# Optimization experiments

Measured on AMD Instinct MI355X. Metric: run time of the kernel, lower is better.

## Reference

```python
import jax, jax.numpy as jnp
import numpy as np

N, E, F, H, L, G = 100000, 1600000, 32, 64, 4, 256
EPS = 1e-5


def setup_inputs() -> dict:
    key = jax.random.key(0)
    ks = jax.random.split(key, 12)
    x = jax.random.normal(ks[0], (N, F), dtype=jnp.float32)
    edge_index = jax.random.randint(ks[1], (2, E), 0, N, dtype=jnp.int32)
    batch = jnp.sort(jax.random.randint(ks[2], (N,), 0, G, dtype=jnp.int32))
    s = 0.1
    return {
        "x": x,
        "edge_index": edge_index,
        "batch": batch,
        "w_embed": jax.random.normal(ks[3], (F, H), dtype=jnp.float32) * s,
        "b_embed": jnp.zeros((H,), dtype=jnp.float32),
        "conv_W": jax.random.normal(ks[4], (L, H, H), dtype=jnp.float32) * s,
        "conv_b": jnp.zeros((L, H), dtype=jnp.float32),
        "bn_gamma": jnp.ones((L, H), dtype=jnp.float32),
        "bn_beta": jnp.zeros((L, H), dtype=jnp.float32),
        "w1": jax.random.normal(ks[5], (H, H // 2), dtype=jnp.float32) * s,
        "b1": jnp.zeros((H // 2,), dtype=jnp.float32),
        "w2": jax.random.normal(ks[6], (H // 2, 1), dtype=jnp.float32) * s,
        "b2": jnp.zeros((1,), dtype=jnp.float32),
    }


def _gcn_conv(h, src, dst, W, b):
    # PyG GCNConv: add self loops, symmetric D^-1/2 (A+I) D^-1/2 normalization
    hw = h @ W  # [N,H]
    deg = jax.ops.segment_sum(jnp.ones((E,), h.dtype), dst, num_segments=N) + 1.0
    dinv = jax.lax.rsqrt(deg)  # [N]
    msg = hw[src] * (dinv[src] * dinv[dst])[:, None]  # [E,H] gather + scale
    agg = jax.ops.segment_sum(msg, dst, num_segments=N)  # scatter-add
    agg = agg + hw * (dinv * dinv)[:, None]  # self-loop contribution
    return agg + b


def _batchnorm(h, gamma, beta):
    # training-mode BatchNorm1d over the node dimension
    mean = jnp.mean(h, axis=0)
    var = jnp.var(h, axis=0)
    return (h - mean) * jax.lax.rsqrt(var + EPS) * gamma + beta


def reference(x, edge_index, batch, w_embed, b_embed, conv_W, conv_b,
              bn_gamma, bn_beta, w1, b1, w2, b2):
    src, dst = edge_index[0], edge_index[1]
    h = x @ w_embed + b_embed  # node embedding [N,H]
    for i in range(L):
        identity = h
        h = _gcn_conv(h, src, dst, conv_W[i], conv_b[i])
        h = _batchnorm(h, bn_gamma[i], bn_beta[i])
        h = jax.nn.relu(h)
        # dropout is identity in eval mode
        h = h + identity  # use_residual=True
    # global mean pool over graphs
    sums = jax.ops.segment_sum(h, batch, num_segments=G)  # [G,H]
    counts = jax.ops.segment_sum(jnp.ones((N,), h.dtype), batch, num_segments=G)
    pooled = sums / jnp.maximum(counts, 1.0)[:, None]
    out = jax.nn.relu(pooled @ w1 + b1)
    out = out @ w2 + b2  # [G,1]
    return out
```

## Files before the change

### kernel.cpp

```cpp
#include <hip/hip_runtime.h>
#include <hip/hip_fp16.h>

#define Nn 100000
#define Ne 1600000
#define Fi 32
#define Hd 64
#define Ll 4
#define Gg 256
#define BN_EPS 1e-5f
#define NPB 128
#define NBINS ((Nn + NPB - 1) / NPB)
#define CHUNK 4096
#define NBLK ((Ne + CHUNK - 1) / CHUNK)
#define IDXW (NBINS + 2)
#define TPAD 68
#define XPAD 36
#define NGB ((Nn + 63) / 64)
#define NSH 128
#define WSZ 256


__global__ void k_scanA(const int* __restrict__ deg, int* __restrict__ row_off,
                        int* __restrict__ bsum) {
    __shared__ int s[256];
    int t = threadIdx.x;
    int i = blockIdx.x * 256 + t;
    int v = (i < Nn) ? deg[i] : 0;
    s[t] = v;
    __syncthreads();
    int x = v;
    for (int off = 1; off < 256; off <<= 1) {
        int u = (t >= off) ? s[t - off] : 0;
        __syncthreads();
        x += u;
        s[t] = x;
        __syncthreads();
    }
    if (i < Nn) row_off[i] = x - v;
    if (t == 255) bsum[blockIdx.x] = x;
}

__global__ void k_scanBG(int* __restrict__ bsum, int nblk,
                         const int* __restrict__ batch, int* __restrict__ gstart) {
    int t = threadIdx.x;
    if (blockIdx.x == 1) {
        if (t < Gg) {
            int lo = 0, hi = Nn;
            while (lo < hi) {
                int mid = (lo + hi) >> 1;
                if (batch[mid] < t) lo = mid + 1; else hi = mid;
            }
            gstart[t] = lo;
            if (t == 0) gstart[Gg] = Nn;
        }
        return;
    }
    __shared__ int s[512];
    int v = (t < nblk) ? bsum[t] : 0;
    s[t] = v;
    __syncthreads();
    int x = v;
    for (int off = 1; off < 512; off <<= 1) {
        int u = (t >= off) ? s[t - off] : 0;
        __syncthreads();
        x += u;
        s[t] = x;
        __syncthreads();
    }
    if (t < nblk) bsum[t] = x - v;
}

__global__ void k_scanC(int* __restrict__ row_off, const int* __restrict__ bsum,
                        const int* __restrict__ deg, float* __restrict__ dinv) {
    int i = blockIdx.x * 256 + threadIdx.x;
    if (i < Nn) {
        row_off[i] += bsum[blockIdx.x];
        dinv[i] = rsqrtf((float)deg[i] + 1.0f);
    }
    if (i == 0) row_off[Nn] = Ne;
}

__global__ __launch_bounds__(256) void k_part(const int* __restrict__ src,
                                              const int* __restrict__ dst,
                                              unsigned* __restrict__ tpack,
                                              unsigned short* __restrict__ idx16) {
    __shared__ int hist[NBINS];
    __shared__ int lofs[NBINS + 1];
    __shared__ int wsum[256];
    __shared__ unsigned stage[CHUNK];
    int blk = blockIdx.x, t = threadIdx.x;
    int e0 = blk * CHUNK;
    int nval = min(CHUNK, Ne - e0);

    for (int i = t; i < NBINS; i += 256) hist[i] = 0;
    __syncthreads();
    for (int i = t; i < nval; i += 256)
        atomicAdd(&hist[dst[e0 + i] >> 7], 1);
    __syncthreads();

    int base = t * 4;
    int loc[4];
    int s = 0;
#pragma unroll
    for (int k = 0; k < 4; k++) {
        int b = base + k;
        int c = (b < NBINS) ? hist[b] : 0;
        loc[k] = s;
        s += c;
    }
    wsum[t] = s;
    __syncthreads();
    int x = s;
    for (int off = 1; off < 256; off <<= 1) {
        int u = (t >= off) ? wsum[t - off] : 0;
        __syncthreads();
        x += u;
        wsum[t] = x;
        __syncthreads();
    }
    int excl = x - s;
#pragma unroll
    for (int k = 0; k < 4; k++) {
        int b = base + k;
        if (b < NBINS) lofs[b] = excl + loc[k];
    }
    if (t == 0) lofs[NBINS] = nval;
    __syncthreads();

    for (int i = t; i <= NBINS; i += 256)
        idx16[(size_t)blk * IDXW + i] = (unsigned short)lofs[i];

    for (int i = t; i < NBINS; i += 256) hist[i] = lofs[i];
    __syncthreads();
    for (int i = t; i < nval; i += 256) {
        int d = dst[e0 + i];
        int sv = src[e0 + i];
        int p = atomicAdd(&hist[d >> 7], 1);
        stage[p] = (unsigned)sv | ((unsigned)(d & (NPB - 1)) << 17);
    }
    __syncthreads();
    for (int i = t; i < nval; i += 256)
        tpack[(size_t)blk * CHUNK + i] = stage[i];
}

__global__ __launch_bounds__(256) void k_deg2(const unsigned* __restrict__ tpack,
                                              const unsigned short* __restrict__ idx16,
                                              int* __restrict__ deg) {
    __shared__ int cnt[NPB];
    int b = blockIdx.x, t = threadIdx.x;
    if (t < NPB) cnt[t] = 0;
    __syncthreads();
    for (int r = t; r < NBLK; r += 256) {
        const unsigned short* row = idx16 + (size_t)r * IDXW;
        int s = row[b], e = row[b + 1];
        const unsigned* tp = tpack + (size_t)r * CHUNK;
        for (int k = s; k < e; k++)
            atomicAdd(&cnt[tp[k] >> 17], 1);
    }
    __syncthreads();
    int node = b * NPB + t;
    if (t < NPB && node < Nn) deg[node] = cnt[t];
}

__global__ __launch_bounds__(256) void k_csr(const int* __restrict__ row_off,
                                             const unsigned* __restrict__ tpack,
                                             const unsigned short* __restrict__ idx16,
                                             int* __restrict__ esrc) {
    __shared__ int cur[NPB];
    int b = blockIdx.x, t = threadIdx.x;
    int n0 = b * NPB;
    int e0 = row_off[n0];
    if (t < NPB) {
        int node = n0 + t;
        cur[t] = (node < Nn) ? (row_off[node] - e0) : 0;
    }
    __syncthreads();
    for (int r = t; r < NBLK; r += 256) {
        const unsigned short* row = idx16 + (size_t)r * IDXW;
        int s = row[b], e = row[b + 1];
        const unsigned* tp = tpack + (size_t)r * CHUNK;
        for (int k = s; k < e; k++) {
            unsigned v = tp[k];
            int p = atomicAdd(&cur[v >> 17], 1);
            esrc[e0 + p] = (int)(v & 0x1FFFFu);
        }
    }
}


#define MT_FMA(AV, W0, W1, W2, W3, R)                                          \
    acc[R][0] = fmaf(AV.x, W0.x, acc[R][0]);                                   \
    acc[R][0] = fmaf(AV.y, W1.x, acc[R][0]);                                   \
    acc[R][0] = fmaf(AV.z, W2.x, acc[R][0]);                                   \
    acc[R][0] = fmaf(AV.w, W3.x, acc[R][0]);                                   \
    acc[R][1] = fmaf(AV.x, W0.y, acc[R][1]);                                   \
    acc[R][1] = fmaf(AV.y, W1.y, acc[R][1]);                                   \
    acc[R][1] = fmaf(AV.z, W2.y, acc[R][1]);                                   \
    acc[R][1] = fmaf(AV.w, W3.y, acc[R][1]);                                   \
    acc[R][2] = fmaf(AV.x, W0.z, acc[R][2]);                                   \
    acc[R][2] = fmaf(AV.y, W1.z, acc[R][2]);                                   \
    acc[R][2] = fmaf(AV.z, W2.z, acc[R][2]);                                   \
    acc[R][2] = fmaf(AV.w, W3.z, acc[R][2]);                                   \
    acc[R][3] = fmaf(AV.x, W0.w, acc[R][3]);                                   \
    acc[R][3] = fmaf(AV.y, W1.w, acc[R][3]);                                   \
    acc[R][3] = fmaf(AV.z, W2.w, acc[R][3]);                                   \
    acc[R][3] = fmaf(AV.w, W3.w, acc[R][3]);

__device__ inline void store_half4(unsigned short* dst, float a, float b,
                                   float c, float d) {
    __half2 p0 = __floats2half2_rn(a, b);
    __half2 p1 = __floats2half2_rn(c, d);
    uint2 u;
    u.x = *(unsigned*)&p0;
    u.y = *(unsigned*)&p1;
    *(uint2*)dst = u;
}

__global__ __launch_bounds__(256, 4) void k_gemmF2(const float* __restrict__ agg,
                                                   const float* __restrict__ bnacc,
                                                   const float* __restrict__ gamma,
                                                   const float* __restrict__ beta,
                                                   float* __restrict__ h,
                                                   const float* __restrict__ W,
                                                   const float* __restrict__ dinv,
                                                   unsigned short* __restrict__ hwh) {
    __shared__ float hs[64 * TPAD];
    __shared__ float ws[64 * 64];
    __shared__ float bsc[64], bsh[64];
    int t = threadIdx.x;
    int n0 = blockIdx.x * 64;

    for (int f = t; f < 1024; f += 256)
        ((float4*)ws)[f] = ((const float4*)W)[f];

    if (t < 64) {
        float s = 0.f, s2 = 0.f;
        for (int shd = 0; shd < NSH; shd++) {
            s  += bnacc[shd * 128 + t];
            s2 += bnacc[shd * 128 + 64 + t];
        }
        float mean = s / (float)Nn;
        float var = fmaxf(s2 / (float)Nn - mean * mean, 0.f);
        float scv = gamma[t] * rsqrtf(var + BN_EPS);
        bsc[t] = scv;
        bsh[t] = beta[t] - mean * scv;
    }
    __syncthreads();

    for (int f = t; f < 1024; f += 256) {
        int row = f >> 4, c4 = (f & 15) * 4;
        int node = n0 + row;
        if (node < Nn) {
            float4 a  = *(const float4*)(agg + (size_t)node * Hd + c4);
            float4 ho = *(const float4*)(h + (size_t)node * Hd + c4);
            float4 sc = ((const float4*)bsc)[f & 15];
            float4 sh = ((const float4*)bsh)[f & 15];
            float4 r4;
            r4.x = fmaxf(fmaf(a.x, sc.x, sh.x), 0.f) + ho.x;
            r4.y = fmaxf(fmaf(a.y, sc.y, sh.y), 0.f) + ho.y;
            r4.z = fmaxf(fmaf(a.z, sc.z, sh.z), 0.f) + ho.z;
            r4.w = fmaxf(fmaf(a.w, sc.w, sh.w), 0.f) + ho.w;
            *(float4*)(h + (size_t)node * Hd + c4) = r4;
            *(float4*)&hs[row * TPAD + c4] = r4;
        } else {
            *(float4*)&hs[row * TPAD + c4] = make_float4(0.f, 0.f, 0.f, 0.f);
        }
    }
    __syncthreads();

    int i = t >> 4, j = t & 15;
    float acc[4][4] = {};
#pragma unroll 2
    for (int k = 0; k < 64; k += 4) {
        float4 w0 = *(const float4*)&ws[(k + 0) * 64 + 4 * j];
        float4 w1 = *(const float4*)&ws[(k + 1) * 64 + 4 * j];
        float4 w2 = *(const float4*)&ws[(k + 2) * 64 + 4 * j];
        float4 w3 = *(const float4*)&ws[(k + 3) * 64 + 4 * j];
        float4 a0 = *(const float4*)&hs[(4 * i + 0) * TPAD + k];
        float4 a1 = *(const float4*)&hs[(4 * i + 1) * TPAD + k];
        float4 a2 = *(const float4*)&hs[(4 * i + 2) * TPAD + k];
        float4 a3 = *(const float4*)&hs[(4 * i + 3) * TPAD + k];
        MT_FMA(a0, w0, w1, w2, w3, 0)
        MT_FMA(a1, w0, w1, w2, w3, 1)
        MT_FMA(a2, w0, w1, w2, w3, 2)
        MT_FMA(a3, w0, w1, w2, w3, 3)
    }
#pragma unroll
    for (int r = 0; r < 4; r++) {
        int node = n0 + 4 * i + r;
        if (node < Nn) {
            float dv = dinv[node];
            store_half4(hwh + (size_t)node * Hd + 4 * j,
                        acc[r][0] * dv, acc[r][1] * dv, acc[r][2] * dv,
                        acc[r][3] * dv);
        }
    }
}

__global__ __launch_bounds__(256, 4) void k_embed_gemm2(const float* __restrict__ x,
                                                        const float* __restrict__ we,
                                                        const float* __restrict__ be,
                                                        const float* __restrict__ W,
                                                        float* __restrict__ h,
                                                        const float* __restrict__ dinv,
                                                        unsigned short* __restrict__ hwh) {
    __shared__ float uni[64 * XPAD + 32 * 64];
    __shared__ float hs[64 * TPAD];
    __shared__ float bes[64];
    float* xs  = uni;
    float* wes = uni + 64 * XPAD;
    float* ws  = uni;
    int t = threadIdx.x;
    int n0 = blockIdx.x * 64;

    for (int f = t; f < 512; f += 256)
        ((float4*)wes)[f] = ((const float4*)we)[f];
    if (t < 64) bes[t] = be[t];

    for (int f = t; f < 512; f += 256) {
        int row = f >> 3, c4 = (f & 7) * 4;
        int node = n0 + row;
        float4 v = (node < Nn) ? *(const float4*)(x + (size_t)node * Fi + c4)
                               : make_float4(0.f, 0.f, 0.f, 0.f);
        *(float4*)&xs[row * XPAD + c4] = v;
    }
    __syncthreads();

    int i = t >> 4, j = t & 15;
    {
        float acc[4][4];
#pragma unroll
        for (int r = 0; r < 4; r++)
#pragma unroll
            for (int c = 0; c < 4; c++) acc[r][c] = bes[4 * j + c];
#pragma unroll 2
        for (int k = 0; k < 32; k += 4) {
            float4 w0 = *(const float4*)&wes[(k + 0) * 64 + 4 * j];
            float4 w1 = *(const float4*)&wes[(k + 1) * 64 + 4 * j];
            float4 w2 = *(const float4*)&wes[(k + 2) * 64 + 4 * j];
            float4 w3 = *(const float4*)&wes[(k + 3) * 64 + 4 * j];
            float4 a0 = *(const float4*)&xs[(4 * i + 0) * XPAD + k];
            float4 a1 = *(const float4*)&xs[(4 * i + 1) * XPAD + k];
            float4 a2 = *(const float4*)&xs[(4 * i + 2) * XPAD + k];
            float4 a3 = *(const float4*)&xs[(4 * i + 3) * XPAD + k];
            MT_FMA(a0, w0, w1, w2, w3, 0)
            MT_FMA(a1, w0, w1, w2, w3, 1)
            MT_FMA(a2, w0, w1, w2, w3, 2)
            MT_FMA(a3, w0, w1, w2, w3, 3)
        }
#pragma unroll
        for (int r = 0; r < 4; r++) {
            int node = n0 + 4 * i + r;
            float4 hv = make_float4(acc[r][0], acc[r][1], acc[r][2], acc[r][3]);
            *(float4*)&hs[(4 * i + r) * TPAD + 4 * j] = hv;
            if (node < Nn)
                *(float4*)(h + (size_t)node * Hd + 4 * j) = hv;
        }
    }
    __syncthreads();
    for (int f = t; f < 1024; f += 256)
        ((float4*)ws)[f] = ((const float4*)W)[f];
    __syncthreads();
    {
        float acc[4][4] = {};
#pragma unroll 2
        for (int k = 0; k < 64; k += 4) {
            float4 w0 = *(const float4*)&ws[(k + 0) * 64 + 4 * j];
            float4 w1 = *(const float4*)&ws[(k + 1) * 64 + 4 * j];
            float4 w2 = *(const float4*)&ws[(k + 2) * 64 + 4 * j];
            float4 w3 = *(const float4*)&ws[(k + 3) * 64 + 4 * j];
            float4 a0 = *(const float4*)&hs[(4 * i + 0) * TPAD + k];
            float4 a1 = *(const float4*)&hs[(4 * i + 1) * TPAD + k];
            float4 a2 = *(const float4*)&hs[(4 * i + 2) * TPAD + k];
            float4 a3 = *(const float4*)&hs[(4 * i + 3) * TPAD + k];
            MT_FMA(a0, w0, w1, w2, w3, 0)
            MT_FMA(a1, w0, w1, w2, w3, 1)
            MT_FMA(a2, w0, w1, w2, w3, 2)
            MT_FMA(a3, w0, w1, w2, w3, 3)
        }
#pragma unroll
        for (int r = 0; r < 4; r++) {
            int node = n0 + 4 * i + r;
            if (node < Nn) {
                float dv = dinv[node];
                store_half4(hwh + (size_t)node * Hd + 4 * j,
                            acc[r][0] * dv, acc[r][1] * dv, acc[r][2] * dv,
                            acc[r][3] * dv);
            }
        }
    }
}


__global__ __launch_bounds__(256) void k_gatherH(const unsigned short* __restrict__ hwh,
                                                 const float* __restrict__ dinv,
                                                 const int* __restrict__ row_off,
                                                 const int* __restrict__ esrc,
                                                 const float* __restrict__ bias,
                                                 float* __restrict__ agg,
                                                 float* __restrict__ bnacc) {
    __shared__ int se[4][WSZ];
    __shared__ float ls[2048];
    int t = threadIdx.x;
    int w = t >> 6, lane = t & 63;
    int g = lane >> 3, l = lane & 7;
    int node = blockIdx.x * 32 + w * 8 + g;
    float di = dinv[node];
    int en0 = row_off[node], en1 = row_off[node + 1];
    int we0 = __shfl(en0, 0, 64);
    int we1 = __shfl(en1, 63, 64);

    float acc[8];
    uint4 v = *(const uint4*)(hwh + (size_t)node * Hd + l * 8);
#pragma unroll
    for (int q = 0; q < 4; q++) {
        float2 f = __half22float2(*(__half2*)(((unsigned*)&v) + q));
        acc[2 * q]     = f.x;
        acc[2 * q + 1] = f.y;
    }

    for (int wb = we0; wb < we1; wb += WSZ) {
        int cnt = min(WSZ, we1 - wb);
        for (int k2 = lane; k2 < cnt; k2 += 64)
            se[w][k2] = esrc[wb + k2];
        __builtin_amdgcn_wave_barrier();
        asm volatile("s_waitcnt lgkmcnt(0)" ::: "memory");
        int j  = max(en0, wb) - wb;
        int j1 = min(en1, wb + cnt) - wb;
        for (; j + 7 < j1; j += 8) {
            uint4 vv[8];
#pragma unroll
            for (int u = 0; u < 8; u++)
                vv[u] = *(const uint4*)(hwh + (size_t)se[w][j + u] * Hd + l * 8);
#pragma unroll
            for (int u = 0; u < 8; u++) {
#pragma unroll
                for (int q = 0; q < 4; q++) {
                    float2 f = __half22float2(*(__half2*)(((unsigned*)&vv[u]) + q));
                    acc[2 * q]     += f.x;
                    acc[2 * q + 1] += f.y;
                }
            }
        }
        for (; j < j1; j++) {
            uint4 v0 = *(const uint4*)(hwh + (size_t)se[w][j] * Hd + l * 8);
#pragma unroll
            for (int q = 0; q < 4; q++) {
                float2 f = __half22float2(*(__half2*)(((unsigned*)&v0) + q));
                acc[2 * q]     += f.x;
                acc[2 * q + 1] += f.y;
            }
        }
        __builtin_amdgcn_wave_barrier();
    }

#pragma unroll
    for (int q = 0; q < 8; q++)
        acc[q] = fmaf(acc[q], di, bias[l * 8 + q]);

    *(float4*)(agg + (size_t)node * Hd + l * 8)     = make_float4(acc[0], acc[1], acc[2], acc[3]);
    *(float4*)(agg + (size_t)node * Hd + l * 8 + 4) = make_float4(acc[4], acc[5], acc[6], acc[7]);

    int g32 = t >> 3;
    *(float4*)&ls[g32 * 64 + l * 8]     = make_float4(acc[0], acc[1], acc[2], acc[3]);
    *(float4*)&ls[g32 * 64 + l * 8 + 4] = make_float4(acc[4], acc[5], acc[6], acc[7]);
    __syncthreads();
    if (t < 64) {
        float s = 0.f, s2 = 0.f;
#pragma unroll
        for (int gg = 0; gg < 32; gg++) {
            float vv = ls[gg * 64 + t];
            s += vv;
            s2 = fmaf(vv, vv, s2);
        }
        float* a = bnacc + (blockIdx.x & (NSH - 1)) * 128;
        atomicAdd(&a[t], s);
        atomicAdd(&a[64 + t], s2);
    }
}

__global__ __launch_bounds__(1024) void k_poolF(const float* __restrict__ agg,
                                                const float* __restrict__ bnacc,
                                                const float* __restrict__ gamma,
                                                const float* __restrict__ beta,
                                                const float* __restrict__ h,
                                                const int* __restrict__ gstart,
                                                float* __restrict__ pooled) {
    __shared__ float ls[1024];
    __shared__ float bsc[64], bsh[64];
    int g = blockIdx.x;
    int t = threadIdx.x;
    if (t < 64) {
        float s = 0.f, s2 = 0.f;
        for (int shd = 0; shd < NSH; shd++) {
            s  += bnacc[shd * 128 + t];
            s2 += bnacc[shd * 128 + 64 + t];
        }
        float mean = s / (float)Nn;
        float var = fmaxf(s2 / (float)Nn - mean * mean, 0.f);
        float scv = gamma[t] * rsqrtf(var + BN_EPS);
        bsc[t] = scv;
        bsh[t] = beta[t] - mean * scv;
    }
    __syncthreads();
    int ch = t & 63, sl = t >> 6;
    float sc = bsc[ch], shv = bsh[ch];
    int n0 = gstart[g], n1 = gstart[g + 1];
    float s = 0.f;
    for (int n = n0 + sl; n < n1; n += 16) {
        float a  = agg[(size_t)n * Hd + ch];
        float ho = h[(size_t)n * Hd + ch];
        s += fmaxf(fmaf(a, sc, shv), 0.f) + ho;
    }
    ls[t] = s;
    __syncthreads();
    if (t < 64) {
        float acc = 0.f;
#pragma unroll
        for (int k = 0; k < 16; k++) acc += ls[k * 64 + t];
        float cnt = (float)(n1 - n0);
        pooled[g * Hd + t] = acc / fmaxf(cnt, 1.0f);
    }
}

__global__ __launch_bounds__(256) void k_head(const float* __restrict__ pooled,
                                              const float* __restrict__ w1,
                                              const float* __restrict__ b1,
                                              const float* __restrict__ w2,
                                              const float* __restrict__ b2,
                                              float* __restrict__ out) {
    __shared__ float sw1[Hd * 32], sw2[32], sb1[32];
    int t = threadIdx.x;
    for (int i = t; i < Hd * 32; i += 256) sw1[i] = w1[i];
    if (t < 32) { sw2[t] = w2[t]; sb1[t] = b1[t]; }
    __syncthreads();
    float acc2[32];
#pragma unroll
    for (int k = 0; k < 32; k++) acc2[k] = sb1[k];
    for (int j = 0; j < Hd; j++) {
        float pj = pooled[t * Hd + j];
#pragma unroll
        for (int k = 0; k < 32; k++) acc2[k] = fmaf(pj, sw1[j * 32 + k], acc2[k]);
    }
    float o = b2[0];
#pragma unroll
    for (int k = 0; k < 32; k++) o += fmaxf(acc2[k], 0.f) * sw2[k];
    out[t] = o;
}


extern "C" void kernel_launch(void* const* d_in, const int* in_sizes, int n_in,
                              void* d_out, int out_size, void* d_ws, size_t ws_size,
                              hipStream_t stream) {
    const float* x       = (const float*)d_in[0];
    const int*   eidx    = (const int*)d_in[1];
    const int*   batch   = (const int*)d_in[2];
    const float* w_embed = (const float*)d_in[3];
    const float* b_embed = (const float*)d_in[4];
    const float* conv_W  = (const float*)d_in[5];
    const float* conv_b  = (const float*)d_in[6];
    const float* gamma   = (const float*)d_in[7];
    const float* beta    = (const float*)d_in[8];
    const float* w1      = (const float*)d_in[9];
    const float* b1      = (const float*)d_in[10];
    const float* w2      = (const float*)d_in[11];
    const float* b2      = (const float*)d_in[12];
    const int* src = eidx;
    const int* dst = eidx + Ne;

    char* p = (char*)d_ws;
    auto alloc = [&](size_t bytes) -> void* {
        void* r = (void*)p;
        p += (bytes + 255) / 256 * 256;
        return r;
    };
    float*    h       = (float*)alloc((size_t)Nn * Hd * 4);
    unsigned short* hwh = (unsigned short*)alloc((size_t)Nn * Hd * 2);
    float*    agg     = (float*)alloc((size_t)Nn * Hd * 4);
    int*      deg     = (int*)alloc((size_t)Nn * 4);
    int*      row_off = (int*)alloc((size_t)(Nn + 1) * 4);
    float*    dinv    = (float*)alloc((size_t)Nn * 4);
    int*      bsum    = (int*)alloc(512 * 4);
    int*      esrc    = (int*)alloc((size_t)Ne * 4);
    unsigned* tpack   = (unsigned*)alloc((size_t)NBLK * CHUNK * 4);
    unsigned short* idx16 = (unsigned short*)alloc((size_t)NBLK * IDXW * 2);
    float*    bnacc   = (float*)alloc((size_t)Ll * NSH * 128 * 4);
    float*    pooled  = (float*)alloc((size_t)Gg * Hd * 4);
    int*      gstart  = (int*)alloc((size_t)(Gg + 1) * 4);
    (void)ws_size; (void)in_sizes; (void)n_in; (void)out_size;

    const int NB_N = (Nn + 255) / 256;
    const int NB_G32 = Nn / 32;

    hipMemsetAsync(bnacc, 0, (size_t)Ll * NSH * 128 * 4, stream);

    k_part<<<NBLK, 256, 0, stream>>>(src, dst, tpack, idx16);
    k_deg2<<<NBINS, 256, 0, stream>>>(tpack, idx16, deg);
    k_scanA<<<NB_N, 256, 0, stream>>>(deg, row_off, bsum);
    k_scanBG<<<2, 512, 0, stream>>>(bsum, NB_N, batch, gstart);
    k_scanC<<<NB_N, 256, 0, stream>>>(row_off, bsum, deg, dinv);
    k_csr<<<NBINS, 256, 0, stream>>>(row_off, tpack, idx16, esrc);

    k_embed_gemm2<<<NGB, 256, 0, stream>>>(x, w_embed, b_embed, conv_W, h, dinv, hwh);

    for (int i = 0; i < Ll; i++) {
        if (i > 0)
            k_gemmF2<<<NGB, 256, 0, stream>>>(agg, bnacc + (size_t)(i - 1) * NSH * 128,
                                              gamma + (size_t)(i - 1) * Hd,
                                              beta + (size_t)(i - 1) * Hd, h,
                                              conv_W + (size_t)i * Hd * Hd, dinv, hwh);
        k_gatherH<<<NB_G32, 256, 0, stream>>>(hwh, dinv, row_off, esrc,
                                              conv_b + (size_t)i * Hd, agg,
                                              bnacc + (size_t)i * NSH * 128);
    }

    k_poolF<<<Gg, 1024, 0, stream>>>(agg, bnacc + (size_t)(Ll - 1) * NSH * 128,
                                     gamma + (size_t)(Ll - 1) * Hd,
                                     beta + (size_t)(Ll - 1) * Hd, h, gstart, pooled);
    k_head<<<1, 256, 0, stream>>>(pooled, w1, b1, w2, b2, (float*)d_out);
}
```

Baseline: 346.4 us.

## Split hidden features into 16-wide slabs and gather each slab in a separate pass

```diff
diff --git a/kernel.cpp b/kernel.cpp
--- a/kernel.cpp
+++ b/kernel.cpp
@@ -17,7 +17,7 @@
 #define XPAD 36
 #define NGB ((Nn + 63) / 64)
 #define NSH 128
-#define WSZ 256
+#define NB_GQ ((Nn + 127) / 128)
 
 
 __global__ void k_scanA(const int* __restrict__ deg, int* __restrict__ row_off,
@@ -216,6 +216,10 @@
     *(uint2*)dst = u;
 }
 
+__device__ inline unsigned short* hwh_addr(unsigned short* hwh, int node, int j) {
+    return hwh + ((size_t)(j >> 2) * Nn + node) * 16 + 4 * (j & 3);
+}
+
 __global__ __launch_bounds__(256, 4) void k_gemmF2(const float* __restrict__ agg,
                                                    const float* __restrict__ bnacc,
                                                    const float* __restrict__ gamma,
@@ -290,7 +294,7 @@
         int node = n0 + 4 * i + r;
         if (node < Nn) {
             float dv = dinv[node];
-            store_half4(hwh + (size_t)node * Hd + 4 * j,
+            store_half4(hwh_addr(hwh, node, j),
                         acc[r][0] * dv, acc[r][1] * dv, acc[r][2] * dv,
                         acc[r][3] * dv);
         }
@@ -383,7 +387,7 @@
             int node = n0 + 4 * i + r;
             if (node < Nn) {
                 float dv = dinv[node];
-                store_half4(hwh + (size_t)node * Hd + 4 * j,
+                store_half4(hwh_addr(hwh, node, j),
                             acc[r][0] * dv, acc[r][1] * dv, acc[r][2] * dv,
                             acc[r][3] * dv);
             }
@@ -392,90 +396,79 @@
 }
 
 
-__global__ __launch_bounds__(256) void k_gatherH(const unsigned short* __restrict__ hwh,
+__global__ __launch_bounds__(256) void k_gather4(const unsigned short* __restrict__ hwq,
                                                  const float* __restrict__ dinv,
                                                  const int* __restrict__ row_off,
                                                  const int* __restrict__ esrc,
                                                  const float* __restrict__ bias,
                                                  float* __restrict__ agg,
-                                                 float* __restrict__ bnacc) {
-    __shared__ int se[4][WSZ];
-    __shared__ float ls[2048];
+                                                 float* __restrict__ bnacc,
+                                                 int q) {
+    __shared__ float ls[128 * 16];
     int t = threadIdx.x;
-    int w = t >> 6, lane = t & 63;
-    int g = lane >> 3, l = lane & 7;
-    int node = blockIdx.x * 32 + w * 8 + g;
-    float di = dinv[node];
-    int en0 = row_off[node], en1 = row_off[node + 1];
-    int we0 = __shfl(en0, 0, 64);
-    int we1 = __shfl(en1, 63, 64);
-
-    float acc[8];
-    uint4 v = *(const uint4*)(hwh + (size_t)node * Hd + l * 8);
-#pragma unroll
-    for (int q = 0; q < 4; q++) {
-        float2 f = __half22float2(*(__half2*)(((unsigned*)&v) + q));
-        acc[2 * q]     = f.x;
-        acc[2 * q + 1] = f.y;
-    }
-
-    for (int wb = we0; wb < we1; wb += WSZ) {
-        int cnt = min(WSZ, we1 - wb);
-        for (int k2 = lane; k2 < cnt; k2 += 64)
-            se[w][k2] = esrc[wb + k2];
-        __builtin_amdgcn_wave_barrier();
-        asm volatile("s_waitcnt lgkmcnt(0)" ::: "memory");
-        int j  = max(en0, wb) - wb;
-        int j1 = min(en1, wb + cnt) - wb;
-        for (; j + 7 < j1; j += 8) {
+    int slot = t >> 1, half = t & 1;
+    int node = blockIdx.x * 128 + slot;
+    float acc[8] = {0.f, 0.f, 0.f, 0.f, 0.f, 0.f, 0.f, 0.f};
+
+    if (node < Nn) {
+        float di = dinv[node];
+        uint4 v = *(const uint4*)(hwq + (size_t)node * 16 + half * 8);
+#pragma unroll
+        for (int k = 0; k < 4; k++) {
+            float2 f = __half22float2(*(__half2*)(((unsigned*)&v) + k));
+            acc[2 * k]     = f.x;
+            acc[2 * k + 1] = f.y;
+        }
+        int e = row_off[node], e1 = row_off[node + 1];
+        for (; e + 7 < e1; e += 8) {
             uint4 vv[8];
 #pragma unroll
             for (int u = 0; u < 8; u++)
-                vv[u] = *(const uint4*)(hwh + (size_t)se[w][j + u] * Hd + l * 8);
+                vv[u] = *(const uint4*)(hwq + (size_t)esrc[e + u] * 16 + half * 8);
 #pragma unroll
             for (int u = 0; u < 8; u++) {
 #pragma unroll
-                for (int q = 0; q < 4; q++) {
-                    float2 f = __half22float2(*(__half2*)(((unsigned*)&vv[u]) + q));
-                    acc[2 * q]     += f.x;
-                    acc[2 * q + 1] += f.y;
+                for (int k = 0; k < 4; k++) {
+                    float2 f = __half22float2(*(__half2*)(((unsigned*)&vv[u]) + k));
+                    acc[2 * k]     += f.x;
+                    acc[2 * k + 1] += f.y;
                 }
             }
         }
-        for (; j < j1; j++) {
-            uint4 v0 = *(const uint4*)(hwh + (size_t)se[w][j] * Hd + l * 8);
-#pragma unroll
-            for (int q = 0; q < 4; q++) {
-                float2 f = __half22float2(*(__half2*)(((unsigned*)&v0) + q));
-                acc[2 * q]     += f.x;
-                acc[2 * q + 1] += f.y;
+        for (; e < e1; e++) {
+            uint4 v0 = *(const uint4*)(hwq + (size_t)esrc[e] * 16 + half * 8);
+#pragma unroll
+            for (int k = 0; k < 4; k++) {
+                float2 f = __half22float2(*(__half2*)(((unsigned*)&v0) + k));
+                acc[2 * k]     += f.x;
+                acc[2 * k + 1] += f.y;
             }
         }
-        __builtin_amdgcn_wave_barrier();
-    }
-
-#pragma unroll
-    for (int q = 0; q < 8; q++)
-        acc[q] = fmaf(acc[q], di, bias[l * 8 + q]);
-
-    *(float4*)(agg + (size_t)node * Hd + l * 8)     = make_float4(acc[0], acc[1], acc[2], acc[3]);
-    *(float4*)(agg + (size_t)node * Hd + l * 8 + 4) = make_float4(acc[4], acc[5], acc[6], acc[7]);
-
-    int g32 = t >> 3;
-    *(float4*)&ls[g32 * 64 + l * 8]     = make_float4(acc[0], acc[1], acc[2], acc[3]);
-    *(float4*)&ls[g32 * 64 + l * 8 + 4] = make_float4(acc[4], acc[5], acc[6], acc[7]);
-    __syncthreads();
-    if (t < 64) {
+#pragma unroll
+        for (int k = 0; k < 8; k++)
+            acc[k] = fmaf(acc[k], di, bias[q * 16 + half * 8 + k]);
+        *(float4*)(agg + (size_t)node * Hd + q * 16 + half * 8)     =
+            make_float4(acc[0], acc[1], acc[2], acc[3]);
+        *(float4*)(agg + (size_t)node * Hd + q * 16 + half * 8 + 4) =
+            make_float4(acc[4], acc[5], acc[6], acc[7]);
+    } else {
+#pragma unroll
+        for (int k = 0; k < 8; k++) acc[k] = 0.f;
+    }
+
+    *(float4*)&ls[slot * 16 + half * 8]     = make_float4(acc[0], acc[1], acc[2], acc[3]);
+    *(float4*)&ls[slot * 16 + half * 8 + 4] = make_float4(acc[4], acc[5], acc[6], acc[7]);
+    __syncthreads();
+    if (t < 16) {
         float s = 0.f, s2 = 0.f;
-#pragma unroll
-        for (int gg = 0; gg < 32; gg++) {
-            float vv = ls[gg * 64 + t];
+        for (int n2 = 0; n2 < 128; n2++) {
+            float vv = ls[n2 * 16 + t];
             s += vv;
             s2 = fmaf(vv, vv, s2);
         }
         float* a = bnacc + (blockIdx.x & (NSH - 1)) * 128;
-        atomicAdd(&a[t], s);
-        atomicAdd(&a[64 + t], s2);
+        atomicAdd(&a[q * 16 + t], s);
+        atomicAdd(&a[64 + q * 16 + t], s2);
     }
 }
 
@@ -590,7 +583,6 @@
     (void)ws_size; (void)in_sizes; (void)n_in; (void)out_size;
 
     const int NB_N = (Nn + 255) / 256;
-    const int NB_G32 = Nn / 32;
 
     hipMemsetAsync(bnacc, 0, (size_t)Ll * NSH * 128 * 4, stream);
 
@@ -609,9 +601,11 @@
                                               gamma + (size_t)(i - 1) * Hd,
                                               beta + (size_t)(i - 1) * Hd, h,
                                               conv_W + (size_t)i * Hd * Hd, dinv, hwh);
-        k_gatherH<<<NB_G32, 256, 0, stream>>>(hwh, dinv, row_off, esrc,
-                                              conv_b + (size_t)i * Hd, agg,
-                                              bnacc + (size_t)i * NSH * 128);
+        for (int q = 0; q < 4; q++)
+            k_gather4<<<NB_GQ, 256, 0, stream>>>(hwh + (size_t)q * Nn * 16, dinv,
+                                                 row_off, esrc,
+                                                 conv_b + (size_t)i * Hd, agg,
+                                                 bnacc + (size_t)i * NSH * 128, q);
     }
 
     k_poolF<<<Gg, 1024, 0, stream>>>(agg, bnacc + (size_t)(Ll - 1) * NSH * 128,
```

Measured after the change: 519.0 us. +49.8%, slower.

## Store hidden state and aggregation buffers in fp16, simplify gather loop

Applied to the files above, without the earlier changes.

```diff
diff --git a/kernel.cpp b/kernel.cpp
--- a/kernel.cpp
+++ b/kernel.cpp
@@ -17,7 +17,6 @@
 #define XPAD 36
 #define NGB ((Nn + 63) / 64)
 #define NSH 128
-#define WSZ 256
 
 
 __global__ void k_scanA(const int* __restrict__ deg, int* __restrict__ row_off,
@@ -216,11 +215,29 @@
     *(uint2*)dst = u;
 }
 
-__global__ __launch_bounds__(256, 4) void k_gemmF2(const float* __restrict__ agg,
+__device__ inline void store_half8(unsigned short* dst, const float* a) {
+    __half2 p0 = __floats2half2_rn(a[0], a[1]);
+    __half2 p1 = __floats2half2_rn(a[2], a[3]);
+    __half2 p2 = __floats2half2_rn(a[4], a[5]);
+    __half2 p3 = __floats2half2_rn(a[6], a[7]);
+    uint4 u;
+    u.x = *(unsigned*)&p0; u.y = *(unsigned*)&p1;
+    u.z = *(unsigned*)&p2; u.w = *(unsigned*)&p3;
+    *(uint4*)dst = u;
+}
+
+__device__ inline float4 load_half4(const unsigned short* p) {
+    uint2 u = *(const uint2*)p;
+    float2 f0 = __half22float2(*(__half2*)&u.x);
+    float2 f1 = __half22float2(*(__half2*)&u.y);
+    return make_float4(f0.x, f0.y, f1.x, f1.y);
+}
+
+__global__ __launch_bounds__(256, 4) void k_gemmF2(const unsigned short* __restrict__ aggh,
                                                    const float* __restrict__ bnacc,
                                                    const float* __restrict__ gamma,
                                                    const float* __restrict__ beta,
-                                                   float* __restrict__ h,
+                                                   unsigned short* __restrict__ hh,
                                                    const float* __restrict__ W,
                                                    const float* __restrict__ dinv,
                                                    unsigned short* __restrict__ hwh) {
@@ -251,8 +268,8 @@
         int row = f >> 4, c4 = (f & 15) * 4;
         int node = n0 + row;
         if (node < Nn) {
-            float4 a  = *(const float4*)(agg + (size_t)node * Hd + c4);
-            float4 ho = *(const float4*)(h + (size_t)node * Hd + c4);
+            float4 a  = load_half4(aggh + (size_t)node * Hd + c4);
+            float4 ho = load_half4(hh + (size_t)node * Hd + c4);
             float4 sc = ((const float4*)bsc)[f & 15];
             float4 sh = ((const float4*)bsh)[f & 15];
             float4 r4;
@@ -260,7 +277,7 @@
             r4.y = fmaxf(fmaf(a.y, sc.y, sh.y), 0.f) + ho.y;
             r4.z = fmaxf(fmaf(a.z, sc.z, sh.z), 0.f) + ho.z;
             r4.w = fmaxf(fmaf(a.w, sc.w, sh.w), 0.f) + ho.w;
-            *(float4*)(h + (size_t)node * Hd + c4) = r4;
+            store_half4(hh + (size_t)node * Hd + c4, r4.x, r4.y, r4.z, r4.w);
             *(float4*)&hs[row * TPAD + c4] = r4;
         } else {
             *(float4*)&hs[row * TPAD + c4] = make_float4(0.f, 0.f, 0.f, 0.f);
@@ -301,7 +318,7 @@
                                                         const float* __restrict__ we,
                                                         const float* __restrict__ be,
                                                         const float* __restrict__ W,
-                                                        float* __restrict__ h,
+                                                        unsigned short* __restrict__ hh,
                                                         const float* __restrict__ dinv,
                                                         unsigned short* __restrict__ hwh) {
     __shared__ float uni[64 * XPAD + 32 * 64];
@@ -354,7 +371,7 @@
             float4 hv = make_float4(acc[r][0], acc[r][1], acc[r][2], acc[r][3]);
             *(float4*)&hs[(4 * i + r) * TPAD + 4 * j] = hv;
             if (node < Nn)
-                *(float4*)(h + (size_t)node * Hd + 4 * j) = hv;
+                store_half4(hh + (size_t)node * Hd + 4 * j, hv.x, hv.y, hv.z, hv.w);
         }
     }
     __syncthreads();
@@ -397,20 +414,14 @@
                                                  const int* __restrict__ row_off,
                                                  const int* __restrict__ esrc,
                                                  const float* __restrict__ bias,
-                                                 float* __restrict__ agg,
+                                                 unsigned short* __restrict__ aggh,
                                                  float* __restrict__ bnacc) {
-    __shared__ int se[4][WSZ];
-    __shared__ float ls[2048];
-    int t = threadIdx.x;
-    int w = t >> 6, lane = t & 63;
-    int g = lane >> 3, l = lane & 7;
-    int node = blockIdx.x * 32 + w * 8 + g;
+    int g = threadIdx.x >> 3;
+    int l = threadIdx.x & 7;
+    int node = blockIdx.x * 32 + g;
     float di = dinv[node];
-    int en0 = row_off[node], en1 = row_off[node + 1];
-    int we0 = __shfl(en0, 0, 64);
-    int we1 = __shfl(en1, 63, 64);
-
     float acc[8];
+
     uint4 v = *(const uint4*)(hwh + (size_t)node * Hd + l * 8);
 #pragma unroll
     for (int q = 0; q < 4; q++) {
@@ -419,52 +430,54 @@
         acc[2 * q + 1] = f.y;
     }
 
-    for (int wb = we0; wb < we1; wb += WSZ) {
-        int cnt = min(WSZ, we1 - wb);
-        for (int k2 = lane; k2 < cnt; k2 += 64)
-            se[w][k2] = esrc[wb + k2];
-        __builtin_amdgcn_wave_barrier();
-        asm volatile("s_waitcnt lgkmcnt(0)" ::: "memory");
-        int j  = max(en0, wb) - wb;
-        int j1 = min(en1, wb + cnt) - wb;
-        for (; j + 7 < j1; j += 8) {
-            uint4 vv[8];
-#pragma unroll
-            for (int u = 0; u < 8; u++)
-                vv[u] = *(const uint4*)(hwh + (size_t)se[w][j + u] * Hd + l * 8);
-#pragma unroll
-            for (int u = 0; u < 8; u++) {
-#pragma unroll
-                for (int q = 0; q < 4; q++) {
-                    float2 f = __half22float2(*(__half2*)(((unsigned*)&vv[u]) + q));
-                    acc[2 * q]     += f.x;
-                    acc[2 * q + 1] += f.y;
-                }
-            }
-        }
-        for (; j < j1; j++) {
-            uint4 v0 = *(const uint4*)(hwh + (size_t)se[w][j] * Hd + l * 8);
+    int e = row_off[node], e1 = row_off[node + 1];
+    for (; e + 7 < e1; e += 8) {
+        uint4 vv[8];
+#pragma unroll
+        for (int u = 0; u < 8; u++)
+            vv[u] = *(const uint4*)(hwh + (size_t)esrc[e + u] * Hd + l * 8);
+#pragma unroll
+        for (int u = 0; u < 8; u++) {
 #pragma unroll
             for (int q = 0; q < 4; q++) {
-                float2 f = __half22float2(*(__half2*)(((unsigned*)&v0) + q));
+                float2 f = __half22float2(*(__half2*)(((unsigned*)&vv[u]) + q));
                 acc[2 * q]     += f.x;
                 acc[2 * q + 1] += f.y;
             }
         }
-        __builtin_amdgcn_wave_barrier();
+    }
+    for (; e + 1 < e1; e += 2) {
+        uint4 v0 = *(const uint4*)(hwh + (size_t)esrc[e] * Hd + l * 8);
+        uint4 v1 = *(const uint4*)(hwh + (size_t)esrc[e + 1] * Hd + l * 8);
+#pragma unroll
+        for (int q = 0; q < 4; q++) {
+            float2 f0 = __half22float2(*(__half2*)(((unsigned*)&v0) + q));
+            float2 f1 = __half22float2(*(__half2*)(((unsigned*)&v1) + q));
+            acc[2 * q]     += f0.x + f1.x;
+            acc[2 * q + 1] += f0.y + f1.y;
+        }
+    }
+    if (e < e1) {
+        uint4 v0 = *(const uint4*)(hwh + (size_t)esrc[e] * Hd + l * 8);
+#pragma unroll
+        for (int q = 0; q < 4; q++) {
+            float2 f0 = __half22float2(*(__half2*)(((unsigned*)&v0) + q));
+            acc[2 * q]     += f0.x;
+            acc[2 * q + 1] += f0.y;
+        }
     }
 
 #pragma unroll
     for (int q = 0; q < 8; q++)
         acc[q] = fmaf(acc[q], di, bias[l * 8 + q]);
 
-    *(float4*)(agg + (size_t)node * Hd + l * 8)     = make_float4(acc[0], acc[1], acc[2], acc[3]);
-    *(float4*)(agg + (size_t)node * Hd + l * 8 + 4) = make_float4(acc[4], acc[5], acc[6], acc[7]);
-
-    int g32 = t >> 3;
-    *(float4*)&ls[g32 * 64 + l * 8]     = make_float4(acc[0], acc[1], acc[2], acc[3]);
-    *(float4*)&ls[g32 * 64 + l * 8 + 4] = make_float4(acc[4], acc[5], acc[6], acc[7]);
-    __syncthreads();
+    store_half8(aggh + (size_t)node * Hd + l * 8, acc);
+
+    __shared__ float ls[2048];
+    *(float4*)&ls[g * 64 + l * 8]     = make_float4(acc[0], acc[1], acc[2], acc[3]);
+    *(float4*)&ls[g * 64 + l * 8 + 4] = make_float4(acc[4], acc[5], acc[6], acc[7]);
+    __syncthreads();
+    int t = threadIdx.x;
     if (t < 64) {
         float s = 0.f, s2 = 0.f;
 #pragma unroll
@@ -479,11 +492,11 @@
     }
 }
 
-__global__ __launch_bounds__(1024) void k_poolF(const float* __restrict__ agg,
+__global__ __launch_bounds__(1024) void k_poolF(const unsigned short* __restrict__ aggh,
                                                 const float* __restrict__ bnacc,
                                                 const float* __restrict__ gamma,
                                                 const float* __restrict__ beta,
-                                                const float* __restrict__ h,
+                                                const unsigned short* __restrict__ hh,
                                                 const int* __restrict__ gstart,
                                                 float* __restrict__ pooled) {
     __shared__ float ls[1024];
@@ -508,8 +521,8 @@
     int n0 = gstart[g], n1 = gstart[g + 1];
     float s = 0.f;
     for (int n = n0 + sl; n < n1; n += 16) {
-        float a  = agg[(size_t)n * Hd + ch];
-        float ho = h[(size_t)n * Hd + ch];
+        float a  = __half2float(((const __half*)aggh)[(size_t)n * Hd + ch]);
+        float ho = __half2float(((const __half*)hh)[(size_t)n * Hd + ch]);
         s += fmaxf(fmaf(a, sc, shv), 0.f) + ho;
     }
     ls[t] = s;
@@ -574,9 +587,9 @@
         p += (bytes + 255) / 256 * 256;
         return r;
     };
-    float*    h       = (float*)alloc((size_t)Nn * Hd * 4);
+    unsigned short* hh  = (unsigned short*)alloc((size_t)Nn * Hd * 2);
     unsigned short* hwh = (unsigned short*)alloc((size_t)Nn * Hd * 2);
-    float*    agg     = (float*)alloc((size_t)Nn * Hd * 4);
+    unsigned short* aggh = (unsigned short*)alloc((size_t)Nn * Hd * 2);
     int*      deg     = (int*)alloc((size_t)Nn * 4);
     int*      row_off = (int*)alloc((size_t)(Nn + 1) * 4);
     float*    dinv    = (float*)alloc((size_t)Nn * 4);
@@ -601,21 +614,21 @@
     k_scanC<<<NB_N, 256, 0, stream>>>(row_off, bsum, deg, dinv);
     k_csr<<<NBINS, 256, 0, stream>>>(row_off, tpack, idx16, esrc);
 
-    k_embed_gemm2<<<NGB, 256, 0, stream>>>(x, w_embed, b_embed, conv_W, h, dinv, hwh);
+    k_embed_gemm2<<<NGB, 256, 0, stream>>>(x, w_embed, b_embed, conv_W, hh, dinv, hwh);
 
     for (int i = 0; i < Ll; i++) {
         if (i > 0)
-            k_gemmF2<<<NGB, 256, 0, stream>>>(agg, bnacc + (size_t)(i - 1) * NSH * 128,
+            k_gemmF2<<<NGB, 256, 0, stream>>>(aggh, bnacc + (size_t)(i - 1) * NSH * 128,
                                               gamma + (size_t)(i - 1) * Hd,
-                                              beta + (size_t)(i - 1) * Hd, h,
+                                              beta + (size_t)(i - 1) * Hd, hh,
                                               conv_W + (size_t)i * Hd * Hd, dinv, hwh);
         k_gatherH<<<NB_G32, 256, 0, stream>>>(hwh, dinv, row_off, esrc,
-                                              conv_b + (size_t)i * Hd, agg,
+                                              conv_b + (size_t)i * Hd, aggh,
                                               bnacc + (size_t)i * NSH * 128);
     }
 
-    k_poolF<<<Gg, 1024, 0, stream>>>(agg, bnacc + (size_t)(Ll - 1) * NSH * 128,
+    k_poolF<<<Gg, 1024, 0, stream>>>(aggh, bnacc + (size_t)(Ll - 1) * NSH * 128,
                                      gamma + (size_t)(Ll - 1) * Hd,
-                                     beta + (size_t)(Ll - 1) * Hd, h, gstart, pooled);
+                                     beta + (size_t)(Ll - 1) * Hd, hh, gstart, pooled);
     k_head<<<1, 256, 0, stream>>>(pooled, w1, b1, w2, b2, (float*)d_out);
 }
```

New measurement: 326.5 us. 5.8% less time.
